# Optimization experiments

Hardware: AMD Instinct MI355X
Metric: run time of the kernel (lower is better)

Reference implementation:

```python
import jax, jax.numpy as jnp
import numpy as np


def setup_inputs() -> dict:
    key = jax.random.key(0)
    ks = jax.random.split(key, 12)
    Tq, Tk, B, H = 1024, 1024, 8, 1024
    inp = {
        "inputs_q": jax.random.normal(ks[0], (Tq, B, H), jnp.float32),
        "inputs_kv": jax.random.normal(ks[1], (Tk, B, H), jnp.float32),
        "w_q": jax.random.normal(ks[2], (H, H), jnp.float32) * 0.02,
        "b_q": jnp.zeros((H,), jnp.float32),
        "w_kv": jax.random.normal(ks[3], (2 * H, H), jnp.float32) * 0.02,
        "b_kv": jnp.zeros((2 * H,), jnp.float32),
        "w_o": jax.random.normal(ks[4], (H, H), jnp.float32) * 0.02,
        "b_o": jnp.zeros((H,), jnp.float32),
        # BatchEnsemble rank-1 factors, initialized near 1
        "r_q": 1.0 + 0.05 * jax.random.normal(ks[5], (B, H), jnp.float32),
        "s_q": 1.0 + 0.05 * jax.random.normal(ks[6], (B, H), jnp.float32),
        "r_kv": 1.0 + 0.05 * jax.random.normal(ks[7], (B, H), jnp.float32),
        "s_kv": 1.0 + 0.05 * jax.random.normal(ks[8], (B, 2 * H), jnp.float32),
        "heads": 16,
    }
    return inp


def be_linear(x, w, b, r, s):
    # x: [T,B,Hin], w: [Hout,Hin], r: [B,Hin], s: [B,Hout]
    return jnp.einsum('tbh,oh->tbo', x * r, w) * s + b


def reference(inputs_q, inputs_kv, w_q, b_q, w_kv, b_kv, w_o, b_o,
              r_q, s_q, r_kv, s_kv, heads):
    Tq, B, H = inputs_q.shape
    Tk = inputs_kv.shape[0]
    hd = H // heads
    scale = hd ** -0.5

    q = be_linear(inputs_q, w_q, b_q, r_q, s_q)          # [Tq,B,H]
    kv = be_linear(inputs_kv, w_kv, b_kv, r_kv, s_kv)    # [Tk,B,2H]

    queries = q.reshape(Tq, B * heads, hd)
    kv = kv.reshape(Tk, B * heads, 2, hd)                # layout: head x {k,v} x hd
    keys = kv[:, :, 0, :]
    values = kv[:, :, 1, :]

    scores = jnp.einsum('qnd,knd->nqk', queries, keys) * scale  # [B*heads,Tq,Tk]
    probs = jax.nn.softmax(scores.astype(jnp.float32), axis=-1).astype(scores.dtype)
    # dropout_prob = 0 / eval: dropout is identity
    ctx = jnp.einsum('nqk,knd->qnd', probs, values).reshape(Tq, B, H)
    out = jnp.einsum('tbh,oh->tbo', ctx, w_o) + b_o      # [Tq,B,H]
    return out
```

## Files before the change

kernel.cpp:

```cpp
#include <hip/hip_runtime.h>
#include <stdint.h>

typedef unsigned short u16;
typedef __bf16 bf16x8 __attribute__((ext_vector_type(8)));
typedef float f32x4 __attribute__((ext_vector_type(4)));

typedef __attribute__((address_space(3))) void lds_void;
typedef const __attribute__((address_space(1))) void gbl_void;
#define GLD_LDS16(g, l) __builtin_amdgcn_global_load_lds((gbl_void*)(g), (lds_void*)(l), 16, 0, 0)

#define BAR_RELAX() asm volatile("s_waitcnt vmcnt(4)\n\ts_barrier" ::: "memory")
#define BAR_FULL()  asm volatile("s_waitcnt vmcnt(0)\n\ts_barrier" ::: "memory")

__device__ __forceinline__ u16 f2bf(float f) {
  unsigned u = __float_as_uint(f);
  u += 0x7fffu + ((u >> 16) & 1u);
  return (u16)(u >> 16);
}

__device__ __forceinline__ unsigned pk2bf(float a, float b) {
  unsigned au = __float_as_uint(a) + 0x8000u;
  unsigned bu = __float_as_uint(b) + 0x8000u;
  return __builtin_amdgcn_perm(bu, au, 0x07060302u);
}

__global__ void k_convert_all(const float* __restrict__ inq, const float* __restrict__ r_q,
                              const float* __restrict__ inkv, const float* __restrict__ r_kv,
                              const float* __restrict__ w_q, const float* __restrict__ w_kv,
                              const float* __restrict__ w_o,
                              u16* __restrict__ Xq, u16* __restrict__ Xkv,
                              u16* __restrict__ Wq, u16* __restrict__ Wkv,
                              u16* __restrict__ Wo) {
  int blk = blockIdx.x;
  const float* src; const float* r = nullptr; u16* dst; int base;
  if (blk < 8192)       { src = inq;  r = r_q;  dst = Xq;  base = 0; }
  else if (blk < 16384) { src = inkv; r = r_kv; dst = Xkv; base = 8192; }
  else if (blk < 17408) { src = w_q;  dst = Wq;  base = 16384; }
  else if (blk < 19456) { src = w_kv; dst = Wkv; base = 17408; }
  else                  { src = w_o;  dst = Wo;  base = 19456; }
  int i4 = ((blk - base) * 256 + threadIdx.x) * 4;
  float4 xv = *(const float4*)(src + i4);
  if (r) {
    int rb = ((i4 >> 10) & 7) * 1024 + (i4 & 1023);
    float4 rv = *(const float4*)(r + rb);
    xv.x *= rv.x; xv.y *= rv.y; xv.z *= rv.z; xv.w *= rv.w;
  }
  unsigned long long pk = (unsigned long long)pk2bf(xv.x, xv.y)
      | ((unsigned long long)pk2bf(xv.z, xv.w) << 32);
  *(unsigned long long*)(dst + i4) = pk;
}

template <int MODE>
__device__ __forceinline__ void gemm_tile(const u16* __restrict__ A, const u16* __restrict__ B,
                                          void* __restrict__ Cout, const float* __restrict__ s,
                                          const float* __restrict__ bias, int N, int K,
                                          float postscale, int bx, int by,
                                          u16* As, u16* Bs, int tid,
                                          u16* __restrict__ vt, int h) {
  const int w = tid >> 6, lane = tid & 63;
  const int quad = lane >> 4, l16 = lane & 15;
  const int n0 = bx * 128, m0 = by * 128;
  const int wm = (w & 1) * 64, wn = (w >> 1) * 64;

  f32x4 acc[4][4] = {};

  int srow[2], scol[2];
#pragma unroll
  for (int i = 0; i < 2; ++i) {
    int p = (w * 2 + i) * 64 + lane;
    int row = p >> 2;
    int cb = (p & 3) ^ ((row >> 1) & 3);
    srow[i] = row; scol[i] = cb * 8;
  }
  int offA[4], offB[4];
#pragma unroll
  for (int t = 0; t < 4; ++t) {
    int ra = wm + t * 16 + l16;
    offA[t] = ra * 32 + ((quad ^ ((ra >> 1) & 3)) * 8);
    int rb = wn + t * 16 + l16;
    offB[t] = rb * 32 + ((quad ^ ((rb >> 1) & 3)) * 8);
  }

#pragma unroll
  for (int st = 0; st < 2; ++st)
#pragma unroll
    for (int i = 0; i < 2; ++i) {
      GLD_LDS16(A + (size_t)(m0 + srow[i]) * K + st * 32 + scol[i],
                As + st * 4096 + (w * 2 + i) * 512);
      GLD_LDS16(B + (size_t)(n0 + srow[i]) * K + st * 32 + scol[i],
                Bs + st * 4096 + (w * 2 + i) * 512);
    }

  int cur = 0, nxt = 2;
#pragma unroll 1
  for (int k0 = 0; k0 < K; k0 += 32) {
    if (k0 + 32 >= K) BAR_FULL(); else BAR_RELAX();

    if (k0 + 64 < K) {
#pragma unroll
      for (int i = 0; i < 2; ++i) {
        GLD_LDS16(A + (size_t)(m0 + srow[i]) * K + (k0 + 64) + scol[i],
                  As + nxt * 4096 + (w * 2 + i) * 512);
        GLD_LDS16(B + (size_t)(n0 + srow[i]) * K + (k0 + 64) + scol[i],
                  Bs + nxt * 4096 + (w * 2 + i) * 512);
      }
    }
    const u16* Ac = As + cur * 4096;
    const u16* Bc = Bs + cur * 4096;
    bf16x8 af[4], bfr[4];
#pragma unroll
    for (int mt = 0; mt < 4; ++mt) af[mt] = *(const bf16x8*)(Ac + offA[mt]);
#pragma unroll
    for (int nt = 0; nt < 4; ++nt) bfr[nt] = *(const bf16x8*)(Bc + offB[nt]);
#pragma unroll
    for (int mt = 0; mt < 4; ++mt)
#pragma unroll
      for (int nt = 0; nt < 4; ++nt)
        acc[mt][nt] = __builtin_amdgcn_mfma_f32_16x16x32_bf16(af[mt], bfr[nt], acc[mt][nt], 0, 0, 0);
    cur = (cur == 2) ? 0 : cur + 1;
    nxt = (nxt == 2) ? 0 : nxt + 1;
  }

#pragma unroll
  for (int mt = 0; mt < 4; ++mt)
#pragma unroll
    for (int nt = 0; nt < 4; ++nt) {
      int n = n0 + wn + nt * 16 + l16;
#pragma unroll
      for (int rg = 0; rg < 4; ++rg) {
        int m = m0 + wm + mt * 16 + quad * 4 + rg;
        float v = acc[mt][nt][rg];
        if (MODE == 0) {
          v = (v * s[(m & 7) * N + n] + bias[n]) * postscale;
          ((u16*)Cout)[(size_t)m * N + n] = f2bf(v);
        } else if (MODE == 1) {
          ((float*)Cout)[(size_t)m * N + n] = v + bias[n];
        } else {
          v = v * s[(m & 7) * N + n] + bias[n];
          int b = m & 7, tk = m >> 3;
          int head = b * 16 + h;
          int dloc = nt * 16 + l16;
          if (wn == 0) {
            ((u16*)Cout)[((size_t)(tk * 128 + head)) * 64 + dloc] = f2bf(v);
          } else {
            vt[((size_t)(head * 64 + dloc)) * 1024 + tk] = f2bf(v);
          }
        }
      }
    }
}

__global__ void k_gemm_qkv(const u16* __restrict__ Xq, const u16* __restrict__ Wq,
                           u16* __restrict__ qout, const float* __restrict__ s_q,
                           const float* __restrict__ b_q, float qscale,
                           const u16* __restrict__ Xkv, const u16* __restrict__ Wkv,
                           u16* __restrict__ kbuf, const float* __restrict__ s_kv,
                           const float* __restrict__ b_kv, u16* __restrict__ vt) {
  __shared__ __align__(16) u16 As[3 * 4096];
  __shared__ __align__(16) u16 Bs[3 * 4096];
  const int blk = blockIdx.x;
  const int xcd = blk & 7;
  const int slot = blk >> 3;
  const int bx = slot % 24;
  const int by = xcd * 8 + slot / 24;
  if (bx < 8)
    gemm_tile<0>(Xq, Wq, qout, s_q, b_q, 1024, 1024, qscale, bx, by, As, Bs,
                 threadIdx.x, nullptr, 0);
  else
    gemm_tile<2>(Xkv, Wkv, kbuf, s_kv, b_kv, 2048, 1024, 1.0f, bx - 8, by, As, Bs,
                 threadIdx.x, vt, bx - 8);
}

__global__ void k_gemm_o(const u16* __restrict__ A, const u16* __restrict__ B,
                         float* __restrict__ Cout, const float* __restrict__ bias) {
  __shared__ __align__(16) u16 As[3 * 4096];
  __shared__ __align__(16) u16 Bs[3 * 4096];
  const int blk = blockIdx.x;
  const int xcd = blk & 7;
  const int slot = blk >> 3;
  const int bx = slot % 8;
  const int by = xcd * 8 + slot / 8;
  gemm_tile<1>(A, B, Cout, nullptr, bias, 1024, 1024, 1.0f, bx, by, As, Bs,
               threadIdx.x, nullptr, 0);
}

__global__ __launch_bounds__(256, 3) void k_attn(const u16* __restrict__ qb,
                                                 const u16* __restrict__ kb,
                                                 const u16* __restrict__ vtb,
                                                 u16* __restrict__ ctx) {
  __shared__ __align__(16) u16 Ks[2][4096];
  __shared__ __align__(16) u16 Vts[2][4096];
  __shared__ __align__(16) u16 Ps[4][32 * 72];

  const int tid = threadIdx.x;
  const int w = tid >> 6, lane = tid & 63;
  const int quad = lane >> 4, l16 = lane & 15;
  const int n = blockIdx.x & 127;
  const int q0 = (blockIdx.x >> 7) << 7;
  const int qw = q0 + w * 32;

  bf16x8 bq[2][2];
#pragma unroll
  for (int g = 0; g < 2; ++g)
#pragma unroll
    for (int ks = 0; ks < 2; ++ks)
      bq[g][ks] = *(const bf16x8*)(qb + ((size_t)(qw + g * 16 + l16) * 128 + n) * 64 + ks * 32 + quad * 8);

  const bool isK = (w < 2);
  const int wv = w & 1;
  const u16* gbase[4];
  u16* lbase[4];
#pragma unroll
  for (int i = 0; i < 4; ++i) {
    int p = (wv * 4 + i) * 64 + lane;
    int r = p >> 3;
    int scb = ((p & 7) ^ (r & 7)) * 8;
    if (isK) {
      gbase[i] = kb + ((size_t)r * 128 + n) * 64 + scb;
      lbase[i] = &Ks[0][(wv * 4 + i) * 512];
    } else {
      gbase[i] = vtb + ((size_t)n * 64 + r) * 1024 + scb;
      lbase[i] = &Vts[0][(wv * 4 + i) * 512];
    }
  }
  const size_t gstep = isK ? 8192 : 1;
  const int lstep = 4096;

  float l_i[2] = {0.f, 0.f};
  f32x4 accO[2][4] = {};
  u16* myP = Ps[w];

#pragma unroll
  for (int i = 0; i < 4; ++i) GLD_LDS16(gbase[i], lbase[i]);

#pragma unroll 1
  for (int tk0 = 0; tk0 < 1024; tk0 += 64) {
    const int cur = (tk0 >> 6) & 1;
    __syncthreads();
    if (tk0 < 960) {
      size_t goff = (size_t)(tk0 + 64) * gstep;
#pragma unroll
      for (int i = 0; i < 4; ++i)
        GLD_LDS16(gbase[i] + goff, lbase[i] + (cur ^ 1) * lstep);
    }
    const u16* Kc = Ks[cur];
    const u16* Vc = Vts[cur];

    f32x4 accS[2][4] = {};
#pragma unroll
    for (int mt = 0; mt < 4; ++mt) {
      int r = mt * 16 + l16;
#pragma unroll
      for (int ks = 0; ks < 2; ++ks) {
        bf16x8 ak = *(const bf16x8*)(Kc + r * 64 + (((ks * 4 + quad) ^ (r & 7)) << 3));
#pragma unroll
        for (int g = 0; g < 2; ++g)
          accS[g][mt] = __builtin_amdgcn_mfma_f32_16x16x32_bf16(ak, bq[g][ks], accS[g][mt], 0, 0, 0);
      }
    }

#pragma unroll
    for (int g = 0; g < 2; ++g) {
      float pv[16];
      float ss = 0.f;
#pragma unroll
      for (int mt = 0; mt < 4; ++mt)
#pragma unroll
        for (int rg = 0; rg < 4; ++rg) {
          float p = __builtin_amdgcn_exp2f(accS[g][mt][rg]);
          pv[mt * 4 + rg] = p;
          ss += p;
        }
      ss += __shfl_xor(ss, 16);
      ss += __shfl_xor(ss, 32);
      l_i[g] += ss;
      const int prow = (g * 16 + l16) * 72;
#pragma unroll
      for (int mt = 0; mt < 4; ++mt) {
        unsigned long long pk = (unsigned long long)pk2bf(pv[mt * 4 + 0], pv[mt * 4 + 1])
            | ((unsigned long long)pk2bf(pv[mt * 4 + 2], pv[mt * 4 + 3]) << 32);
        *(unsigned long long*)(myP + prow + mt * 16 + quad * 4) = pk;
      }
    }

    bf16x8 bp[2][2];
#pragma unroll
    for (int g = 0; g < 2; ++g)
#pragma unroll
      for (int ks = 0; ks < 2; ++ks)
        bp[g][ks] = *(const bf16x8*)(myP + (g * 16 + l16) * 72 + ks * 32 + quad * 8);
#pragma unroll
    for (int dt = 0; dt < 4; ++dt) {
      int r = dt * 16 + l16;
#pragma unroll
      for (int ks = 0; ks < 2; ++ks) {
        bf16x8 av = *(const bf16x8*)(Vc + r * 64 + (((ks * 4 + quad) ^ (r & 7)) << 3));
#pragma unroll
        for (int g = 0; g < 2; ++g)
          accO[g][dt] = __builtin_amdgcn_mfma_f32_16x16x32_bf16(av, bp[g][ks], accO[g][dt], 0, 0, 0);
      }
    }
  }

#pragma unroll
  for (int g = 0; g < 2; ++g) {
    float inv = 1.f / l_i[g];
    const size_t obase = ((size_t)(qw + g * 16 + l16) * 128 + n) * 64;
#pragma unroll
    for (int dt = 0; dt < 4; ++dt) {
      unsigned long long pk = (unsigned long long)pk2bf(accO[g][dt][0] * inv, accO[g][dt][1] * inv)
          | ((unsigned long long)pk2bf(accO[g][dt][2] * inv, accO[g][dt][3] * inv) << 32);
      *(unsigned long long*)(ctx + obase + dt * 16 + quad * 4) = pk;
    }
  }
}

extern "C" void kernel_launch(void* const* d_in, const int* in_sizes, int n_in,
                              void* d_out, int out_size, void* d_ws, size_t ws_size,
                              hipStream_t stream) {
  const float* inq  = (const float*)d_in[0];
  const float* inkv = (const float*)d_in[1];
  const float* w_q  = (const float*)d_in[2];
  const float* b_q  = (const float*)d_in[3];
  const float* w_kv = (const float*)d_in[4];
  const float* b_kv = (const float*)d_in[5];
  const float* w_o  = (const float*)d_in[6];
  const float* b_o  = (const float*)d_in[7];
  const float* r_q  = (const float*)d_in[8];
  const float* s_q  = (const float*)d_in[9];
  const float* r_kv = (const float*)d_in[10];
  const float* s_kv = (const float*)d_in[11];

  const size_t MEG = 1024 * 1024;
  u16* ws    = (u16*)d_ws;
  u16* Xq    = ws;
  u16* Xkv   = ws + 8 * MEG;
  u16* Wq    = ws + 16 * MEG;
  u16* Wkv   = ws + 17 * MEG;
  u16* Wo    = ws + 19 * MEG;
  u16* qbuf  = ws + 20 * MEG;
  u16* kbuf  = ws + 28 * MEG;
  u16* vt    = ws + 36 * MEG;
  u16* ctx   = Xq;

  k_convert_all<<<20480, 256, 0, stream>>>(inq, r_q, inkv, r_kv, w_q, w_kv, w_o,
                                           Xq, Xkv, Wq, Wkv, Wo);

  const float QSCALE = 0.125f * 1.44269504088896340736f;
  k_gemm_qkv<<<1536, 256, 0, stream>>>(Xq, Wq, qbuf, s_q, b_q, QSCALE,
                                       Xkv, Wkv, kbuf, s_kv, b_kv, vt);
  k_attn<<<1024, 256, 0, stream>>>(qbuf, kbuf, vt, ctx);
  k_gemm_o<<<512, 256, 0, stream>>>(ctx, Wo, (float*)d_out, b_o);
}
```

Measured before the change: 296.8 us.

## Rewrite QKV projection GEMM with 256x256 tiles and phased async pipeline

Replaces the 128x128-tile QKV GEMM with a 256x256-tile kernel using 512 threads, double-buffered LDS with swizzled layout, and a four-phase schedule that interleaves global-to-LDS loads with MFMA bursts under raised wave priority. Larger tiles raise arithmetic intensity and cut global traffic per FLOP, while the phased barriers are meant to overlap memory with compute. The trade-offs are higher register and LDS use per block, fewer blocks (384) to fill the GPU, and more barriers per K-step.

```diff
diff --git a/kernel.cpp b/kernel.cpp
--- a/kernel.cpp
+++ b/kernel.cpp
@@ -11,6 +11,8 @@
 
 #define BAR_RELAX() asm volatile("s_waitcnt vmcnt(4)\n\ts_barrier" ::: "memory")
 #define BAR_FULL()  asm volatile("s_waitcnt vmcnt(0)\n\ts_barrier" ::: "memory")
+#define BAR()   asm volatile("s_barrier" ::: "memory")
+#define VMW(n)  asm volatile("s_waitcnt vmcnt(" #n ")" ::: "memory")
 
 __device__ __forceinline__ u16 f2bf(float f) {
   unsigned u = __float_as_uint(f);
@@ -50,6 +52,145 @@
   *(unsigned long long*)(dst + i4) = pk;
 }
 
+template <class F0, class F1, class F2, class F3>
+__device__ __forceinline__ void four_phases(const u16* AsT, const u16* BsT,
+                                            int rowA, int rowB, int bof0, int bof1,
+                                            f32x4 (&acc)[8][4],
+                                            F0 st0, F1 st1, F2 st2, F3 st3, bool drain) {
+  bf16x8 bfr[4][2];
+#pragma unroll
+  for (int nt = 0; nt < 4; ++nt) {
+    bfr[nt][0] = *(const bf16x8*)(BsT + rowB + (nt << 10) + bof0);
+    bfr[nt][1] = *(const bf16x8*)(BsT + rowB + (nt << 10) + bof1);
+  }
+#pragma unroll
+  for (int q = 0; q < 4; ++q) {
+    bf16x8 af[2][2];
+#pragma unroll
+    for (int j = 0; j < 2; ++j) {
+      af[j][0] = *(const bf16x8*)(AsT + rowA + ((2 * q + j) << 10) + bof0);
+      af[j][1] = *(const bf16x8*)(AsT + rowA + ((2 * q + j) << 10) + bof1);
+    }
+    if (q == 0) st0(); else if (q == 1) st1(); else if (q == 2) st2(); else st3();
+    BAR();
+    __builtin_amdgcn_s_setprio(1);
+#pragma unroll
+    for (int j = 0; j < 2; ++j)
+#pragma unroll
+      for (int nt = 0; nt < 4; ++nt) {
+        acc[2 * q + j][nt] = __builtin_amdgcn_mfma_f32_16x16x32_bf16(af[j][0], bfr[nt][0], acc[2 * q + j][nt], 0, 0, 0);
+        acc[2 * q + j][nt] = __builtin_amdgcn_mfma_f32_16x16x32_bf16(af[j][1], bfr[nt][1], acc[2 * q + j][nt], 0, 0, 0);
+      }
+    __builtin_amdgcn_s_setprio(0);
+    if (q == 3) { if (drain) VMW(0); else VMW(6); }
+    BAR();
+  }
+}
+
+template <int MODE>
+__device__ __forceinline__ void gemm256(const u16* __restrict__ Amat, const u16* __restrict__ Bmat,
+                                        void* __restrict__ Cout, const float* __restrict__ s,
+                                        const float* __restrict__ bias, int N, float postscale,
+                                        int bx, int by,
+                                        u16* As0, u16* As1, u16* Bs0, u16* Bs1,
+                                        int tid, u16* __restrict__ vt) {
+  const int w = tid >> 6, lane = tid & 63;
+  const int quad = lane >> 4, l16 = lane & 15;
+  const int wm = w & 1, wn = w >> 1;
+  const int m0 = by << 8, n0g = bx << 8;
+
+  const int thr_row = (w << 3) + (lane >> 3);
+  const int sblk = (lane & 7) ^ ((lane >> 3) & 7);
+
+  auto STG = [&](u16* lds, const u16* mat, int rowbase, int k0, int row0) {
+    GLD_LDS16(mat + (size_t)(rowbase + row0 + thr_row) * 1024 + k0 + (sblk << 3),
+              lds + ((row0 + (w << 3)) << 6));
+  };
+
+  const int sw = l16 & 7;
+  const int bof0 = (quad ^ sw) << 3;
+  const int bof1 = ((4 | quad) ^ sw) << 3;
+  const int rowA = ((wm << 7) + l16) << 6;
+  const int rowB = ((wn << 6) + l16) << 6;
+
+  f32x4 acc[8][4] = {};
+
+  STG(As0, Amat, m0, 0, 0);    STG(As0, Amat, m0, 0, 128);
+  STG(As0, Amat, m0, 0, 64);   STG(As0, Amat, m0, 0, 192);
+  STG(Bs0, Bmat, n0g, 0, 0);   STG(Bs0, Bmat, n0g, 0, 64);
+  STG(Bs0, Bmat, n0g, 0, 128); STG(Bs0, Bmat, n0g, 0, 192);
+  STG(Bs1, Bmat, n0g, 64, 0);  STG(Bs1, Bmat, n0g, 64, 64);
+  STG(Bs1, Bmat, n0g, 64, 128);STG(Bs1, Bmat, n0g, 64, 192);
+  STG(As1, Amat, m0, 64, 0);   STG(As1, Amat, m0, 64, 128);
+  VMW(6);
+  BAR();
+
+#pragma unroll 1
+  for (int i = 0; i < 8; ++i) {
+    const int k0 = i << 7;
+    const bool more = i < 7;
+    four_phases(As0, Bs0, rowA, rowB, bof0, bof1, acc,
+        [&]{ STG(As1, Amat, m0, k0 + 64, 64);  STG(As1, Amat, m0, k0 + 64, 192); },
+        [&]{ if (more) { STG(Bs0, Bmat, n0g, k0 + 128, 0);   STG(Bs0, Bmat, n0g, k0 + 128, 64); } },
+        [&]{ if (more) { STG(Bs0, Bmat, n0g, k0 + 128, 128); STG(Bs0, Bmat, n0g, k0 + 128, 192); } },
+        [&]{ if (more) { STG(As0, Amat, m0, k0 + 128, 0);    STG(As0, Amat, m0, k0 + 128, 128); } },
+        !more);
+    four_phases(As1, Bs1, rowA, rowB, bof0, bof1, acc,
+        [&]{ if (more) { STG(As0, Amat, m0, k0 + 128, 64);   STG(As0, Amat, m0, k0 + 128, 192); } },
+        [&]{ if (more) { STG(Bs1, Bmat, n0g, k0 + 192, 0);   STG(Bs1, Bmat, n0g, k0 + 192, 64); } },
+        [&]{ if (more) { STG(Bs1, Bmat, n0g, k0 + 192, 128); STG(Bs1, Bmat, n0g, k0 + 192, 192); } },
+        [&]{ if (more) { STG(As1, Amat, m0, k0 + 192, 0);    STG(As1, Amat, m0, k0 + 192, 128); } },
+        false);
+  }
+
+#pragma unroll
+  for (int mt = 0; mt < 8; ++mt)
+#pragma unroll
+    for (int nt = 0; nt < 4; ++nt) {
+      const int n = n0g + (wn << 6) + (nt << 4) + l16;
+#pragma unroll
+      for (int rg = 0; rg < 4; ++rg) {
+        const int m = m0 + (wm << 7) + (mt << 4) + (quad << 2) + rg;
+        float v = acc[mt][nt][rg];
+        if (MODE == 0) {
+          v = (v * s[(m & 7) * N + n] + bias[n]) * postscale;
+          ((u16*)Cout)[(size_t)m * N + n] = f2bf(v);
+        } else {
+          v = v * s[(m & 7) * N + n] + bias[n];
+          const int b = m & 7, tk = m >> 3;
+          const int head = (b << 4) + (n >> 7);
+          const int dloc = n & 63;
+          if (((n >> 6) & 1) == 0)
+            ((u16*)Cout)[((size_t)(tk * 128 + head) << 6) + dloc] = f2bf(v);
+          else
+            vt[((size_t)((head << 6) + dloc) << 10) + tk] = f2bf(v);
+        }
+      }
+    }
+}
+
+__global__ __launch_bounds__(512, 2) void k_gemm_qkv(
+    const u16* __restrict__ Xq, const u16* __restrict__ Wq,
+    u16* __restrict__ qout, const float* __restrict__ s_q,
+    const float* __restrict__ b_q, float qscale,
+    const u16* __restrict__ Xkv, const u16* __restrict__ Wkv,
+    u16* __restrict__ kbuf, const float* __restrict__ s_kv,
+    const float* __restrict__ b_kv, u16* __restrict__ vt) {
+  __shared__ __align__(16) u16 As[2][16384];
+  __shared__ __align__(16) u16 Bs[2][16384];
+  const int blk = blockIdx.x;
+  const int xcd = blk & 7;
+  const int slot = blk >> 3;
+  const int by = xcd * 4 + slot / 12;
+  const int cx = slot % 12;
+  if (cx < 4)
+    gemm256<0>(Xq, Wq, qout, s_q, b_q, 1024, qscale, cx, by,
+               &As[0][0], &As[1][0], &Bs[0][0], &Bs[1][0], threadIdx.x, nullptr);
+  else
+    gemm256<2>(Xkv, Wkv, kbuf, s_kv, b_kv, 2048, 1.0f, cx - 4, by,
+               &As[0][0], &As[1][0], &Bs[0][0], &Bs[1][0], threadIdx.x, vt);
+}
+
 template <int MODE>
 __device__ __forceinline__ void gemm_tile(const u16* __restrict__ A, const u16* __restrict__ B,
                                           void* __restrict__ Cout, const float* __restrict__ s,
@@ -150,27 +291,6 @@
     }
 }
 
-__global__ void k_gemm_qkv(const u16* __restrict__ Xq, const u16* __restrict__ Wq,
-                           u16* __restrict__ qout, const float* __restrict__ s_q,
-                           const float* __restrict__ b_q, float qscale,
-                           const u16* __restrict__ Xkv, const u16* __restrict__ Wkv,
-                           u16* __restrict__ kbuf, const float* __restrict__ s_kv,
-                           const float* __restrict__ b_kv, u16* __restrict__ vt) {
-  __shared__ __align__(16) u16 As[3 * 4096];
-  __shared__ __align__(16) u16 Bs[3 * 4096];
-  const int blk = blockIdx.x;
-  const int xcd = blk & 7;
-  const int slot = blk >> 3;
-  const int bx = slot % 24;
-  const int by = xcd * 8 + slot / 24;
-  if (bx < 8)
-    gemm_tile<0>(Xq, Wq, qout, s_q, b_q, 1024, 1024, qscale, bx, by, As, Bs,
-                 threadIdx.x, nullptr, 0);
-  else
-    gemm_tile<2>(Xkv, Wkv, kbuf, s_kv, b_kv, 2048, 1024, 1.0f, bx - 8, by, As, Bs,
-                 threadIdx.x, vt, bx - 8);
-}
-
 __global__ void k_gemm_o(const u16* __restrict__ A, const u16* __restrict__ B,
                          float* __restrict__ Cout, const float* __restrict__ bias) {
   __shared__ __align__(16) u16 As[3 * 4096];
@@ -347,8 +467,8 @@
                                            Xq, Xkv, Wq, Wkv, Wo);
 
   const float QSCALE = 0.125f * 1.44269504088896340736f;
-  k_gemm_qkv<<<1536, 256, 0, stream>>>(Xq, Wq, qbuf, s_q, b_q, QSCALE,
-                                       Xkv, Wkv, kbuf, s_kv, b_kv, vt);
+  k_gemm_qkv<<<384, 512, 0, stream>>>(Xq, Wq, qbuf, s_q, b_q, QSCALE,
+                                      Xkv, Wkv, kbuf, s_kv, b_kv, vt);
   k_attn<<<1024, 256, 0, stream>>>(qbuf, kbuf, vt, ctx);
   k_gemm_o<<<512, 256, 0, stream>>>(ctx, Wo, (float*)d_out, b_o);
 }
```

Result: slower. 304.5 us (+2.6%).

## Widen QKV GEMM tiles to 128x256 with 512-thread blocks sharing A loads

Applied to the files above, without the earlier changes.

The fused Q/KV projection GEMM now uses 128x256 output tiles computed by 8 waves per block (512 threads), so each A tile staged in LDS is reused across twice as many output columns. The grid drops to 768 blocks, the B staging buffer doubles, and the wait count drops to vmcnt(3) to match three loads per thread per stage. The epilogue head/K/V index mapping is recomputed from n directly. The aim is less redundant global and LDS traffic for A, at the cost of more LDS per block and fewer blocks in flight.

```diff
diff --git a/kernel.cpp b/kernel.cpp
--- a/kernel.cpp
+++ b/kernel.cpp
@@ -9,8 +9,9 @@
 typedef const __attribute__((address_space(1))) void gbl_void;
 #define GLD_LDS16(g, l) __builtin_amdgcn_global_load_lds((gbl_void*)(g), (lds_void*)(l), 16, 0, 0)
 
-#define BAR_RELAX() asm volatile("s_waitcnt vmcnt(4)\n\ts_barrier" ::: "memory")
-#define BAR_FULL()  asm volatile("s_waitcnt vmcnt(0)\n\ts_barrier" ::: "memory")
+#define BAR_RELAX4() asm volatile("s_waitcnt vmcnt(4)\n\ts_barrier" ::: "memory")
+#define BAR_RELAX3() asm volatile("s_waitcnt vmcnt(3)\n\ts_barrier" ::: "memory")
+#define BAR_FULL()   asm volatile("s_waitcnt vmcnt(0)\n\ts_barrier" ::: "memory")
 
 __device__ __forceinline__ u16 f2bf(float f) {
   unsigned u = __float_as_uint(f);
@@ -51,6 +52,126 @@
 }
 
 template <int MODE>
+__device__ __forceinline__ void gemm_tile2(const u16* __restrict__ A, const u16* __restrict__ B,
+                                           void* __restrict__ Cout, const float* __restrict__ s,
+                                           const float* __restrict__ bias, int N, int K,
+                                           float postscale, int bx, int by,
+                                           u16* As, u16* Bs, int tid,
+                                           u16* __restrict__ vt) {
+  const int w = tid >> 6, lane = tid & 63;
+  const int quad = lane >> 4, l16 = lane & 15;
+  const int n0 = bx * 256, m0 = by * 128;
+  const int wm = (w & 1) * 64, wn = (w >> 1) * 64;
+
+  f32x4 acc[4][4] = {};
+
+  const int arow = tid >> 2;
+  const int acol = ((tid & 3) ^ ((arow >> 1) & 3)) * 8;
+  int brow[2], bcol[2];
+#pragma unroll
+  for (int i = 0; i < 2; ++i) {
+    int p = (w * 2 + i) * 64 + lane;
+    int row = p >> 2;
+    brow[i] = row;
+    bcol[i] = ((p & 3) ^ ((row >> 1) & 3)) * 8;
+  }
+  int offA[4], offB[4];
+#pragma unroll
+  for (int t = 0; t < 4; ++t) {
+    int ra = wm + t * 16 + l16;
+    offA[t] = ra * 32 + ((quad ^ ((ra >> 1) & 3)) * 8);
+    int rb = wn + t * 16 + l16;
+    offB[t] = rb * 32 + ((quad ^ ((rb >> 1) & 3)) * 8);
+  }
+
+#pragma unroll
+  for (int st = 0; st < 2; ++st) {
+    GLD_LDS16(A + (size_t)(m0 + arow) * K + st * 32 + acol,
+              As + st * 4096 + w * 512);
+#pragma unroll
+    for (int i = 0; i < 2; ++i)
+      GLD_LDS16(B + (size_t)(n0 + brow[i]) * K + st * 32 + bcol[i],
+                Bs + st * 8192 + (w * 2 + i) * 512);
+  }
+
+  int cur = 0, nxt = 2;
+#pragma unroll 1
+  for (int k0 = 0; k0 < K; k0 += 32) {
+    if (k0 + 32 >= K) BAR_FULL(); else BAR_RELAX3();
+
+    if (k0 + 64 < K) {
+      GLD_LDS16(A + (size_t)(m0 + arow) * K + (k0 + 64) + acol,
+                As + nxt * 4096 + w * 512);
+#pragma unroll
+      for (int i = 0; i < 2; ++i)
+        GLD_LDS16(B + (size_t)(n0 + brow[i]) * K + (k0 + 64) + bcol[i],
+                  Bs + nxt * 8192 + (w * 2 + i) * 512);
+    }
+    const u16* Ac = As + cur * 4096;
+    const u16* Bc = Bs + cur * 8192;
+    bf16x8 af[4], bfr[4];
+#pragma unroll
+    for (int mt = 0; mt < 4; ++mt) af[mt] = *(const bf16x8*)(Ac + offA[mt]);
+#pragma unroll
+    for (int nt = 0; nt < 4; ++nt) bfr[nt] = *(const bf16x8*)(Bc + offB[nt]);
+#pragma unroll
+    for (int mt = 0; mt < 4; ++mt)
+#pragma unroll
+      for (int nt = 0; nt < 4; ++nt)
+        acc[mt][nt] = __builtin_amdgcn_mfma_f32_16x16x32_bf16(af[mt], bfr[nt], acc[mt][nt], 0, 0, 0);
+    cur = (cur == 2) ? 0 : cur + 1;
+    nxt = (nxt == 2) ? 0 : nxt + 1;
+  }
+
+#pragma unroll
+  for (int mt = 0; mt < 4; ++mt)
+#pragma unroll
+    for (int nt = 0; nt < 4; ++nt) {
+      const int n = n0 + wn + nt * 16 + l16;
+#pragma unroll
+      for (int rg = 0; rg < 4; ++rg) {
+        const int m = m0 + wm + mt * 16 + quad * 4 + rg;
+        float v = acc[mt][nt][rg];
+        if (MODE == 0) {
+          v = (v * s[(m & 7) * N + n] + bias[n]) * postscale;
+          ((u16*)Cout)[(size_t)m * N + n] = f2bf(v);
+        } else {
+          v = v * s[(m & 7) * N + n] + bias[n];
+          const int b = m & 7, tk = m >> 3;
+          const int head = (b << 4) + (n >> 7);
+          const int dloc = n & 63;
+          if (((n >> 6) & 1) == 0)
+            ((u16*)Cout)[((size_t)(tk * 128 + head) << 6) + dloc] = f2bf(v);
+          else
+            vt[((size_t)((head << 6) + dloc) << 10) + tk] = f2bf(v);
+        }
+      }
+    }
+}
+
+__global__ __launch_bounds__(512, 4) void k_gemm_qkv(
+    const u16* __restrict__ Xq, const u16* __restrict__ Wq,
+    u16* __restrict__ qout, const float* __restrict__ s_q,
+    const float* __restrict__ b_q, float qscale,
+    const u16* __restrict__ Xkv, const u16* __restrict__ Wkv,
+    u16* __restrict__ kbuf, const float* __restrict__ s_kv,
+    const float* __restrict__ b_kv, u16* __restrict__ vt) {
+  __shared__ __align__(16) u16 As[3 * 4096];
+  __shared__ __align__(16) u16 Bs[3 * 8192];
+  const int blk = blockIdx.x;
+  const int xcd = blk & 7;
+  const int slot = blk >> 3;
+  const int by = xcd * 8 + slot / 12;
+  const int cx = slot % 12;
+  if (cx < 4)
+    gemm_tile2<0>(Xq, Wq, qout, s_q, b_q, 1024, 1024, qscale, cx, by,
+                  As, Bs, threadIdx.x, nullptr);
+  else
+    gemm_tile2<2>(Xkv, Wkv, kbuf, s_kv, b_kv, 2048, 1024, 1.0f, cx - 4, by,
+                  As, Bs, threadIdx.x, vt);
+}
+
+template <int MODE>
 __device__ __forceinline__ void gemm_tile(const u16* __restrict__ A, const u16* __restrict__ B,
                                           void* __restrict__ Cout, const float* __restrict__ s,
                                           const float* __restrict__ bias, int N, int K,
@@ -94,7 +215,7 @@
   int cur = 0, nxt = 2;
 #pragma unroll 1
   for (int k0 = 0; k0 < K; k0 += 32) {
-    if (k0 + 32 >= K) BAR_FULL(); else BAR_RELAX();
+    if (k0 + 32 >= K) BAR_FULL(); else BAR_RELAX4();
 
     if (k0 + 64 < K) {
 #pragma unroll
@@ -150,27 +271,6 @@
     }
 }
 
-__global__ void k_gemm_qkv(const u16* __restrict__ Xq, const u16* __restrict__ Wq,
-                           u16* __restrict__ qout, const float* __restrict__ s_q,
-                           const float* __restrict__ b_q, float qscale,
-                           const u16* __restrict__ Xkv, const u16* __restrict__ Wkv,
-                           u16* __restrict__ kbuf, const float* __restrict__ s_kv,
-                           const float* __restrict__ b_kv, u16* __restrict__ vt) {
-  __shared__ __align__(16) u16 As[3 * 4096];
-  __shared__ __align__(16) u16 Bs[3 * 4096];
-  const int blk = blockIdx.x;
-  const int xcd = blk & 7;
-  const int slot = blk >> 3;
-  const int bx = slot % 24;
-  const int by = xcd * 8 + slot / 24;
-  if (bx < 8)
-    gemm_tile<0>(Xq, Wq, qout, s_q, b_q, 1024, 1024, qscale, bx, by, As, Bs,
-                 threadIdx.x, nullptr, 0);
-  else
-    gemm_tile<2>(Xkv, Wkv, kbuf, s_kv, b_kv, 2048, 1024, 1.0f, bx - 8, by, As, Bs,
-                 threadIdx.x, vt, bx - 8);
-}
-
 __global__ void k_gemm_o(const u16* __restrict__ A, const u16* __restrict__ B,
                          float* __restrict__ Cout, const float* __restrict__ bias) {
   __shared__ __align__(16) u16 As[3 * 4096];
@@ -347,8 +447,8 @@
                                            Xq, Xkv, Wq, Wkv, Wo);
 
   const float QSCALE = 0.125f * 1.44269504088896340736f;
-  k_gemm_qkv<<<1536, 256, 0, stream>>>(Xq, Wq, qbuf, s_q, b_q, QSCALE,
-                                       Xkv, Wkv, kbuf, s_kv, b_kv, vt);
+  k_gemm_qkv<<<768, 512, 0, stream>>>(Xq, Wq, qbuf, s_q, b_q, QSCALE,
+                                      Xkv, Wkv, kbuf, s_kv, b_kv, vt);
   k_attn<<<1024, 256, 0, stream>>>(qbuf, kbuf, vt, ctx);
   k_gemm_o<<<512, 256, 0, stream>>>(ctx, Wo, (float*)d_out, b_o);
 }
```

Measured after the change: 307.8 us. +3.7%, slower.

## Swap MFMA operands to vectorize GEMM epilogue stores and stage V-transpose through LDS

Applied to the files above, without the earlier changes.

Swaps the MFMA A/B operands so each lane holds four consecutive output columns instead of four rows. Epilogue stores can then be packed bf16x4 or float4 writes with float4 scale/bias loads, replacing scattered 2-byte stores. For the V path, results are transposed through a per-wave LDS buffer and written to vt as 16-byte chunks instead of strided scalar stores. This adds a barrier and LDS traffic, and switches bf16 rounding from round-to-nearest-even to pk2bf's round-half-up in the packed paths.

```diff
diff --git a/kernel.cpp b/kernel.cpp
--- a/kernel.cpp
+++ b/kernel.cpp
@@ -116,38 +116,98 @@
     for (int mt = 0; mt < 4; ++mt)
 #pragma unroll
       for (int nt = 0; nt < 4; ++nt)
-        acc[mt][nt] = __builtin_amdgcn_mfma_f32_16x16x32_bf16(af[mt], bfr[nt], acc[mt][nt], 0, 0, 0);
+        acc[mt][nt] = __builtin_amdgcn_mfma_f32_16x16x32_bf16(bfr[nt], af[mt], acc[mt][nt], 0, 0, 0);
     cur = (cur == 2) ? 0 : cur + 1;
     nxt = (nxt == 2) ? 0 : nxt + 1;
   }
 
-#pragma unroll
-  for (int mt = 0; mt < 4; ++mt)
-#pragma unroll
-    for (int nt = 0; nt < 4; ++nt) {
-      int n = n0 + wn + nt * 16 + l16;
-#pragma unroll
-      for (int rg = 0; rg < 4; ++rg) {
-        int m = m0 + wm + mt * 16 + quad * 4 + rg;
-        float v = acc[mt][nt][rg];
-        if (MODE == 0) {
-          v = (v * s[(m & 7) * N + n] + bias[n]) * postscale;
-          ((u16*)Cout)[(size_t)m * N + n] = f2bf(v);
-        } else if (MODE == 1) {
-          ((float*)Cout)[(size_t)m * N + n] = v + bias[n];
-        } else {
-          v = v * s[(m & 7) * N + n] + bias[n];
-          int b = m & 7, tk = m >> 3;
-          int head = b * 16 + h;
-          int dloc = nt * 16 + l16;
-          if (wn == 0) {
-            ((u16*)Cout)[((size_t)(tk * 128 + head)) * 64 + dloc] = f2bf(v);
-          } else {
-            vt[((size_t)(head * 64 + dloc)) * 1024 + tk] = f2bf(v);
-          }
+  if (MODE == 0) {
+#pragma unroll
+    for (int mt = 0; mt < 4; ++mt) {
+      const int m = m0 + wm + mt * 16 + l16;
+      const size_t rowb = (size_t)m * N;
+      const float* srw = s + (m & 7) * N;
+#pragma unroll
+      for (int nt = 0; nt < 4; ++nt) {
+        const int nb = n0 + wn + nt * 16 + quad * 4;
+        float4 sv = *(const float4*)(srw + nb);
+        float4 bv = *(const float4*)(bias + nb);
+        f32x4 a = acc[mt][nt];
+        unsigned long long pk =
+            (unsigned long long)pk2bf((a[0] * sv.x + bv.x) * postscale,
+                                      (a[1] * sv.y + bv.y) * postscale)
+          | ((unsigned long long)pk2bf((a[2] * sv.z + bv.z) * postscale,
+                                       (a[3] * sv.w + bv.w) * postscale) << 32);
+        *(unsigned long long*)((u16*)Cout + rowb + nb) = pk;
+      }
+    }
+  } else if (MODE == 1) {
+#pragma unroll
+    for (int mt = 0; mt < 4; ++mt) {
+      const int m = m0 + wm + mt * 16 + l16;
+      const size_t rowb = (size_t)m * N;
+#pragma unroll
+      for (int nt = 0; nt < 4; ++nt) {
+        const int nb = n0 + wn + nt * 16 + quad * 4;
+        float4 bv = *(const float4*)(bias + nb);
+        f32x4 a = acc[mt][nt];
+        float4 o = {a[0] + bv.x, a[1] + bv.y, a[2] + bv.z, a[3] + bv.w};
+        *(float4*)((float*)Cout + rowb + nb) = o;
+      }
+    }
+  } else {
+    __syncthreads();
+    if (wn == 0) {
+#pragma unroll
+      for (int mt = 0; mt < 4; ++mt) {
+        const int m = m0 + wm + mt * 16 + l16;
+        const int b = m & 7, tk = m >> 3;
+        u16* krow = (u16*)Cout + ((size_t)(tk * 128 + b * 16 + h)) * 64;
+        const float* srw = s + (m & 7) * N;
+#pragma unroll
+        for (int nt = 0; nt < 4; ++nt) {
+          const int nb = n0 + nt * 16 + quad * 4;
+          float4 sv = *(const float4*)(srw + nb);
+          float4 bv = *(const float4*)(bias + nb);
+          f32x4 a = acc[mt][nt];
+          unsigned long long pk =
+              (unsigned long long)pk2bf(a[0] * sv.x + bv.x, a[1] * sv.y + bv.y)
+            | ((unsigned long long)pk2bf(a[2] * sv.z + bv.z, a[3] * sv.w + bv.w) << 32);
+          *(unsigned long long*)(krow + nt * 16 + quad * 4) = pk;
         }
       }
-    }
+    } else {
+      u16* L = As + (w - 2) * 4608;
+#pragma unroll
+      for (int mt = 0; mt < 4; ++mt) {
+        const int m = m0 + wm + mt * 16 + l16;
+        const int b = m & 7;
+        const int tkl = (mt * 16 + l16) >> 3;
+        const float* srw = s + (m & 7) * N;
+#pragma unroll
+        for (int nt = 0; nt < 4; ++nt) {
+          const int nb = n0 + 64 + nt * 16 + quad * 4;
+          float4 sv = *(const float4*)(srw + nb);
+          float4 bv = *(const float4*)(bias + nb);
+          f32x4 a = acc[mt][nt];
+          const int dl = nt * 16 + quad * 4;
+          L[(dl + 0) * 72 + b * 8 + tkl] = f2bf(a[0] * sv.x + bv.x);
+          L[(dl + 1) * 72 + b * 8 + tkl] = f2bf(a[1] * sv.y + bv.y);
+          L[(dl + 2) * 72 + b * 8 + tkl] = f2bf(a[2] * sv.z + bv.z);
+          L[(dl + 3) * 72 + b * 8 + tkl] = f2bf(a[3] * sv.w + bv.w);
+        }
+      }
+      asm volatile("s_waitcnt lgkmcnt(0)" ::: "memory");
+      const int tk0 = by * 16 + (wm >> 3);
+#pragma unroll
+      for (int it = 0; it < 8; ++it) {
+        const int dloc = it * 8 + (lane >> 3);
+        const int b = lane & 7;
+        bf16x8 vchunk = *(const bf16x8*)(L + dloc * 72 + b * 8);
+        *(bf16x8*)(vt + ((size_t)((b * 16 + h) * 64 + dloc)) * 1024 + tk0) = vchunk;
+      }
+    }
+  }
 }
 
 __global__ void k_gemm_qkv(const u16* __restrict__ Xq, const u16* __restrict__ Wq,
```

New measurement: 286.9 us. -3.4%, faster.
